# Kernel optimization log

Measured on AMD Instinct MI355X. Metric: run time of the kernel, lower is better.

## Reference

```python
import jax, jax.numpy as jnp
import numpy as np
from jax import lax

# Static model/config sizes
B, ANG, C, H, NF, NB = 1, 9, 3, 128, 16, 2


def get_freq_position(n):
    """Anti-diagonal frequency bands of an n x n angular-DCT grid (python/static)."""
    bands = []
    for i in range(n):
        bands.append(([i], [0]))
    for j in range(1, n):
        bands.append(([n - 1], [j]))
    for item in bands:
        while item[0][0] > 0 and item[1][0] < n - 1:
            item[0].insert(0, item[0][0] - 1)
            item[1].insert(0, item[1][0] + 1)
    return bands


def dct_mat(n):
    """Orthonormal DCT-II matrix (row k = k-th basis)."""
    k = jnp.arange(n, dtype=jnp.float32)[:, None]
    i = jnp.arange(n, dtype=jnp.float32)[None, :]
    m = jnp.cos(jnp.pi * (i + 0.5) * k / n) * jnp.sqrt(2.0 / n)
    return m.at[0].multiply(1.0 / np.sqrt(2.0))


def conv3d(x, w, b):
    # x: (N, Cin, D, H, W), w: (Cout, Cin, 3, 3, 3)
    y = lax.conv_general_dilated(x, w, (1, 1, 1), 'SAME',
                                 dimension_numbers=('NCDHW', 'OIDHW', 'NCDHW'))
    return y + b[None, :, None, None, None]


def branch(cut, wi, bi, a, wb, bb):
    """init conv + NB ResBlock3D (PReLU -> Conv3d, residual), plus outer skip."""
    y0 = conv3d(cut, wi, bi)
    y = y0
    for k in range(NB):
        r = jnp.where(y >= 0, y, a[k] * y)  # PReLU (single-parameter)
        y = y + conv3d(r, wb[k], bb[k])
    return y0 + y


def setup_inputs() -> dict:
    key = jax.random.key(0)
    ks = jax.random.split(key, 32)

    def nrm(k, shape, s=0.05):
        return jax.random.normal(k, shape, dtype=jnp.float32) * s

    inp = {"x": jax.random.normal(ks[0], (B, ANG, ANG, C, H, H), dtype=jnp.float32)}
    i = 1
    for n in ("dc", "lo", "mi", "hi"):
        inp[f"w_{n}_i"] = nrm(ks[i], (NF, C, 3, 3, 3)); i += 1
        inp[f"b_{n}_i"] = nrm(ks[i], (NF,)); i += 1
        inp[f"a_{n}"] = jnp.full((NB,), 0.25, dtype=jnp.float32)
        inp[f"w_{n}"] = nrm(ks[i], (NB, NF, NF, 3, 3, 3)); i += 1
        inp[f"b_{n}"] = nrm(ks[i], (NB, NF)); i += 1
    inp["w_last"] = nrm(ks[i], (C, NF))  # 1x1 Conv2d, no bias
    return inp


def reference(x, w_dc_i, b_dc_i, a_dc, w_dc, b_dc,
              w_lo_i, b_lo_i, a_lo, w_lo, b_lo,
              w_mi_i, b_mi_i, a_mi, w_mi, b_mi,
              w_hi_i, b_hi_i, a_hi, w_hi, b_hi, w_last):
    b, u, v, c, h, w = x.shape
    Da = dct_mat(u)  # angular DCT (u == v)
    Ds = dct_mat(h)  # spatial DCT (h == w)

    # SpaAngDCT: spatial 2D DCT then angular 2D DCT
    xf = jnp.einsum('buvchw,Hh,Ww->buvcHW', x, Ds, Ds)
    xf = jnp.einsum('buvchw,Uu,Vv->bUVchw', xf, Da, Da)

    x_rec = jnp.zeros((b, NF, u, v, h, w), dtype=x.dtype)
    for idx, (ui, vi) in enumerate(get_freq_position(u)):
        if idx == 0:
            p = (w_dc_i, b_dc_i, a_dc, w_dc, b_dc)
        elif idx <= 2:
            p = (w_lo_i, b_lo_i, a_lo, w_lo, b_lo)
        elif idx <= u - 1:
            p = (w_mi_i, b_mi_i, a_mi, w_mi, b_mi)
        else:
            p = (w_hi_i, b_hi_i, a_hi, w_hi, b_hi)
        ua, va = jnp.array(ui), jnp.array(vi)
        cut = xf[:, ua, va].transpose(0, 2, 1, 3, 4)  # (b, c, L, h, w)
        out = branch(cut, *p)                          # (b, NF, L, h, w)
        x_rec = x_rec.at[:, :, ua, va].set(out)        # scatter band back

    # 'b c u v h w -> b c (u h) (v w)' then 1x1 conv (NF -> 3)
    xr = x_rec.transpose(0, 1, 2, 4, 3, 5).reshape(b, NF, u * h, v * w)
    xr = jnp.einsum('bnHW,on->boHW', xr, w_last)
    xr = xr.reshape(b, c, u, h, v, w).transpose(0, 2, 4, 1, 3, 5)  # (b,u,v,c,h,w)

    # InverseSpaAngDCT: angular IDCT then spatial IDCT
    xr = jnp.einsum('bUVchw,Uu,Vv->buvchw', xr, Da, Da)
    xr = jnp.einsum('buvcHW,Hh,Ww->buvchw', xr, Ds, Ds)
    return xr + x
```

## Files before the change

### kernel.cpp

```cpp
#include <hip/hip_runtime.h>
#include <hip/hip_bf16.h>
#include <math.h>

typedef __hip_bfloat16 bf16;
typedef __attribute__((ext_vector_type(8))) short short8;
typedef __attribute__((ext_vector_type(4))) float floatx4;
typedef __attribute__((ext_vector_type(4))) unsigned int uint4v;
typedef __attribute__((ext_vector_type(2))) unsigned int uint2v;

#define HW 16384
#define NSLICE 243

__constant__ int c_s_of_p[81] = {
  0, 1,1, 2,2,2, 3,3,3,3, 4,4,4,4,4, 5,5,5,5,5,5, 6,6,6,6,6,6,6,
  7,7,7,7,7,7,7,7, 8,8,8,8,8,8,8,8,8, 9,9,9,9,9,9,9,9,
  10,10,10,10,10,10,10, 11,11,11,11,11,11, 12,12,12,12,12,
  13,13,13,13, 14,14,14, 15,15, 16};
__constant__ int c_l_of_p[81] = {
  0, 0,1, 0,1,2, 0,1,2,3, 0,1,2,3,4, 0,1,2,3,4,5, 0,1,2,3,4,5,6,
  0,1,2,3,4,5,6,7, 0,1,2,3,4,5,6,7,8, 0,1,2,3,4,5,6,7,
  0,1,2,3,4,5,6, 0,1,2,3,4,5, 0,1,2,3,4, 0,1,2,3, 0,1,2, 0,1, 0};
__constant__ int c_L_of_s[17] = {1,2,3,4,5,6,7,8,9,8,7,6,5,4,3,2,1};
__constant__ int c_g_of_s[17] = {0,1,1,2,2,2,2,2,2,3,3,3,3,3,3,3,3};
__constant__ int c_pos_uv[81] = {
  0,1,3,6,10,15,21,28,36,
  2,4,7,11,16,22,29,37,45,
  5,8,12,17,23,30,38,46,53,
  9,13,18,24,31,39,47,54,60,
  14,19,25,32,40,48,55,61,66,
  20,26,33,41,49,56,62,67,71,
  27,34,42,50,57,63,68,72,75,
  35,43,51,58,64,69,73,76,78,
  44,52,59,65,70,74,77,79,80};

struct WPtrs {
  const float* wi[4]; const float* bi[4]; const float* a[4];
  const float* wb[4]; const float* bb[4]; const float* wl;
};

__device__ __forceinline__ unsigned short f2bf(float f) {
  return __bfloat16_as_ushort(__float2bfloat16(f));
}
__device__ __forceinline__ float bf2f(unsigned short u) {
  return __uint_as_float(((unsigned int)u) << 16);
}
__device__ __forceinline__ float bflo(unsigned int w) {
  return __uint_as_float(w << 16);
}
__device__ __forceinline__ float bfhi(unsigned int w) {
  return __uint_as_float(w & 0xffff0000u);
}
__device__ __forceinline__ unsigned int pack2(float a, float b) {
  return (unsigned int)f2bf(a) | ((unsigned int)f2bf(b) << 16);
}
__device__ __forceinline__ float invprelu(float v, float invA) {
  return (v >= 0.f) ? v : v * invA;
}
__device__ __forceinline__ void bfsplit(float v, unsigned short& hi, unsigned short& lo) {
  unsigned int bits = __float_as_uint(v);
  hi = (unsigned short)(bits >> 16);
  lo = f2bf(v - __uint_as_float(bits & 0xffff0000u));
}
__device__ __forceinline__ void gl_lds16(const void* g, void* l) {
  __builtin_amdgcn_global_load_lds(
      (const __attribute__((address_space(1))) unsigned int*)g,
      (__attribute__((address_space(3))) unsigned int*)l, 16, 0, 0);
}
__device__ __forceinline__ int ldsoff(int plane, int col) {
  return plane * 2112 + ((plane & 3) << 5) + (col << 4);
}

__global__ __launch_bounds__(256) void k_init(WPtrs P, float* DaF,
                                              unsigned short* TFhi, unsigned short* TFlo,
                                              unsigned short* TIhi, unsigned short* TIlo,
                                              unsigned short* Wmf,
                                              float* BiF, float* BbF,
                                              float* AF, float* WlF) {
  const double PI = 3.14159265358979323846;
  int t = blockIdx.x * 256 + threadIdx.x;
  if (t < 81) {
    int U = t / 9, u = t % 9;
    double d = cos(PI * (u + 0.5) * U / 9.0) * sqrt(2.0 / 9.0);
    if (U == 0) d *= (1.0 / sqrt(2.0));
    DaF[t] = (float)d;
  }
  if (t < 16384) {
    int jj = t & 7, lane = (t >> 3) & 63, ks = (t >> 9) & 3, tile = t >> 11;
    int row = tile * 16 + (lane & 15);
    int colk = ks * 32 + (lane >> 4) * 8 + jj;
    double vF = cos(PI * (colk + 0.5) * row / 128.0) * sqrt(2.0 / 128.0);
    if (row == 0) vF *= (1.0 / sqrt(2.0));
    double vI = cos(PI * (row + 0.5) * colk / 128.0) * sqrt(2.0 / 128.0);
    if (colk == 0) vI *= (1.0 / sqrt(2.0));
    unsigned short h, l;
    bfsplit((float)vF, h, l); TFhi[t] = h; TFlo[t] = l;
    bfsplit((float)vI, h, l); TIhi[t] = h; TIlo[t] = l;
  }
  if (t < 92160) {
    int s = t / 7680, r = t % 7680;
    int step = r / 512, r2 = r % 512;
    int lane = r2 >> 3, j = r2 & 7;
    int d = step / 5, i = step % 5;
    int q = lane >> 4, m = lane & 15;
    int tl = 2 * i + (q >> 1);
    int cin = (q & 1) * 8 + j;
    float val = 0.f;
    if (tl <= 8) {
      int ky = tl / 3, kx = tl % 3;
      int tap = d * 9 + ky * 3 + kx;
      if (s < 4) {
        if (cin < 3) val = P.wi[s][(m * 3 + cin) * 27 + tap];
      } else {
        int g = (s - 4) >> 1, k = (s - 4) & 1;
        val = P.wb[g][((k * 16 + m) * 16 + cin) * 27 + tap];
      }
    }
    Wmf[t] = f2bf(val);
  }
  if (t < 64)  BiF[t] = P.bi[t / 16][t % 16];
  if (t < 128) BbF[t] = P.bb[t / 32][t % 32];
  if (t < 8)   AF[t]  = P.a[t / 2][t % 2];
  if (t < 48)  WlF[t] = P.wl[t];
}

__global__ __launch_bounds__(256) void k_dct2(const float* __restrict__ X,
                                              const unsigned short* __restrict__ tabhi,
                                              const unsigned short* __restrict__ tablo,
                                              const float* __restrict__ xres,
                                              float* __restrict__ Yf,
                                              unsigned short* __restrict__ Ybf) {
  __shared__ unsigned short sThi[128 * 136];
  __shared__ unsigned short sTlo[128 * 136];
  int s = blockIdx.x;
  int t = threadIdx.x;
  int lane = t & 63, wv = t >> 6;
  int q = lane >> 4, n16 = lane & 15;
  const float* Xs = X + (size_t)s * HW;

  floatx4 acc[2][8];
#pragma unroll
  for (int mt = 0; mt < 2; mt++)
#pragma unroll
    for (int nt = 0; nt < 8; nt++) acc[mt][nt] = (floatx4){0.f, 0.f, 0.f, 0.f};

#pragma unroll
  for (int ks = 0; ks < 4; ks++) {
    short8 ahi[2], alo[2];
#pragma unroll
    for (int mt = 0; mt < 2; mt++) {
      const float* xp = Xs + (wv * 32 + mt * 16 + n16) * 128 + ks * 32 + q * 8;
      float4 a = *(const float4*)xp;
      float4 b = *(const float4*)(xp + 4);
      union { short8 v; unsigned short u[8]; } H, L;
      float xv[8] = {a.x, a.y, a.z, a.w, b.x, b.y, b.z, b.w};
#pragma unroll
      for (int j = 0; j < 8; j++) bfsplit(xv[j], H.u[j], L.u[j]);
      ahi[mt] = H.v; alo[mt] = L.v;
    }
#pragma unroll
    for (int nt = 0; nt < 8; nt++) {
      int e = nt * 2048 + ks * 512 + lane * 8;
      short8 bh = *(const short8*)(tabhi + e);
      short8 bl = *(const short8*)(tablo + e);
#pragma unroll
      for (int mt = 0; mt < 2; mt++) {
        acc[mt][nt] = __builtin_amdgcn_mfma_f32_16x16x32_bf16(ahi[mt], bl, acc[mt][nt], 0, 0, 0);
        acc[mt][nt] = __builtin_amdgcn_mfma_f32_16x16x32_bf16(alo[mt], bh, acc[mt][nt], 0, 0, 0);
        acc[mt][nt] = __builtin_amdgcn_mfma_f32_16x16x32_bf16(ahi[mt], bh, acc[mt][nt], 0, 0, 0);
      }
    }
  }

#pragma unroll
  for (int mt = 0; mt < 2; mt++)
#pragma unroll
    for (int nt = 0; nt < 8; nt++) {
      int col = nt * 16 + n16;
      int rowb = wv * 32 + mt * 16 + q * 4;
#pragma unroll
      for (int rp = 0; rp < 4; rp += 2) {
        unsigned short h0, l0, h1, l1;
        bfsplit(acc[mt][nt][rp], h0, l0);
        bfsplit(acc[mt][nt][rp + 1], h1, l1);
        int widx = (col * 136 + rowb + rp) >> 1;
        ((unsigned int*)sThi)[widx] = (unsigned int)h0 | ((unsigned int)h1 << 16);
        ((unsigned int*)sTlo)[widx] = (unsigned int)l0 | ((unsigned int)l1 << 16);
      }
    }
  __syncthreads();

#pragma unroll
  for (int mt = 0; mt < 2; mt++)
#pragma unroll
    for (int nt = 0; nt < 8; nt++) acc[mt][nt] = (floatx4){0.f, 0.f, 0.f, 0.f};

#pragma unroll
  for (int ks = 0; ks < 4; ks++) {
    short8 ahi[2], alo[2];
#pragma unroll
    for (int mt = 0; mt < 2; mt++) {
      int e = (wv * 2 + mt) * 2048 + ks * 512 + lane * 8;
      ahi[mt] = *(const short8*)(tabhi + e);
      alo[mt] = *(const short8*)(tablo + e);
    }
#pragma unroll
    for (int nt = 0; nt < 8; nt++) {
      int off = (nt * 16 + n16) * 136 + ks * 32 + q * 8;
      short8 bh = *(const short8*)(sThi + off);
      short8 bl = *(const short8*)(sTlo + off);
#pragma unroll
      for (int mt = 0; mt < 2; mt++) {
        acc[mt][nt] = __builtin_amdgcn_mfma_f32_16x16x32_bf16(ahi[mt], bl, acc[mt][nt], 0, 0, 0);
        acc[mt][nt] = __builtin_amdgcn_mfma_f32_16x16x32_bf16(alo[mt], bh, acc[mt][nt], 0, 0, 0);
        acc[mt][nt] = __builtin_amdgcn_mfma_f32_16x16x32_bf16(ahi[mt], bh, acc[mt][nt], 0, 0, 0);
      }
    }
  }

#pragma unroll
  for (int mt = 0; mt < 2; mt++)
#pragma unroll
    for (int nt = 0; nt < 8; nt++) {
      int row0 = wv * 32 + mt * 16 + q * 4;
      int col = nt * 16 + n16;
#pragma unroll
      for (int r = 0; r < 4; r++) {
        size_t oi = (size_t)s * HW + (size_t)(row0 + r) * 128 + col;
        float v = acc[mt][nt][r];
        if (Ybf) {
          Ybf[oi] = f2bf(v);
        } else {
          if (xres) v += xres[oi];
          Yf[oi] = v;
        }
      }
    }
}

__global__ __launch_bounds__(256) void k_angfwd(const unsigned short* __restrict__ in,
                                                const float* __restrict__ DaF,
                                                unsigned short* __restrict__ out) {
  __shared__ float sDa[81];
  int t = threadIdx.x;
  if (t < 81) sDa[t] = DaF[t];
  __syncthreads();
  int idx = blockIdx.x * 256 + t;
  int hw = idx & (HW - 1);
  int r = idx >> 14;
  int c = r % 3, ub = r / 3;
  float tmp[3][9];
#pragma unroll
  for (int i = 0; i < 3; i++)
#pragma unroll
    for (int v = 0; v < 9; v++) tmp[i][v] = 0.f;
#pragma unroll
  for (int u = 0; u < 9; u++) {
    float fv[9];
#pragma unroll
    for (int v = 0; v < 9; v++)
      fv[v] = bf2f(in[(size_t)((u * 9 + v) * 3 + c) * HW + hw]);
#pragma unroll
    for (int i = 0; i < 3; i++) {
      float dc = sDa[(ub * 3 + i) * 9 + u];
#pragma unroll
      for (int v = 0; v < 9; v++) tmp[i][v] += dc * fv[v];
    }
  }
#pragma unroll
  for (int i = 0; i < 3; i++) {
    int U = ub * 3 + i;
#pragma unroll
    for (int V = 0; V < 9; V++) {
      float acc = 0.f;
#pragma unroll
      for (int v = 0; v < 9; v++) acc += sDa[V * 9 + v] * tmp[i][v];
      size_t base = ((size_t)c_pos_uv[U * 9 + V] * HW + hw) * 4;
      out[base + c] = f2bf(acc);
      if (c == 0) out[base + 3] = 0;
    }
  }
}

__global__ __launch_bounds__(256) void k_anginv(const float* __restrict__ xrb,
                                                const float* __restrict__ DaF,
                                                float* __restrict__ out) {
  __shared__ float sDa[81];
  int t = threadIdx.x;
  if (t < 81) sDa[t] = DaF[t];
  __syncthreads();
  int idx = blockIdx.x * 256 + t;
  int hw = idx & (HW - 1);
  int r = idx >> 14;
  int c = r % 3, ub = r / 3;
  float tmp[3][9];
#pragma unroll
  for (int i = 0; i < 3; i++)
#pragma unroll
    for (int V = 0; V < 9; V++) tmp[i][V] = 0.f;
#pragma unroll
  for (int U = 0; U < 9; U++) {
    float fV[9];
#pragma unroll
    for (int V = 0; V < 9; V++)
      fV[V] = xrb[((size_t)c_pos_uv[U * 9 + V] * 3 + c) * HW + hw];
#pragma unroll
    for (int i = 0; i < 3; i++) {
      float dc = sDa[U * 9 + (ub * 3 + i)];
#pragma unroll
      for (int V = 0; V < 9; V++) tmp[i][V] += dc * fV[V];
    }
  }
#pragma unroll
  for (int i = 0; i < 3; i++) {
    int u = ub * 3 + i;
#pragma unroll
    for (int v = 0; v < 9; v++) {
      float acc = 0.f;
#pragma unroll
      for (int V = 0; V < 9; V++) acc += sDa[V * 9 + v] * tmp[i][V];
      out[(size_t)((u * 9 + v) * 3 + c) * HW + hw] = acc;
    }
  }
}

__global__ __launch_bounds__(1024, 8) void k_conv(const unsigned short* __restrict__ src,
                                              const unsigned short* __restrict__ prevAct,
                                              const unsigned short* __restrict__ act0,
                                              const unsigned short* __restrict__ Wmf,
                                              const float* __restrict__ BiF,
                                              const float* __restrict__ BbF,
                                              const float* __restrict__ AF,
                                              const float* __restrict__ WlF,
                                              int sel,
                                              unsigned short* __restrict__ boutAct,
                                              float* __restrict__ xrbOut) {
  __shared__ unsigned short s_lds[21184];
  int p = blockIdx.y;
  int s = c_s_of_p[p], l = c_l_of_p[p];
  int g = c_g_of_s[s], Ls = c_L_of_s[s];
  int row0 = blockIdx.x * 8;
  int t = threadIdx.x;
  int lane = t & 63, wv16 = t >> 6;
  int row8 = wv16 & 7, ch = wv16 >> 3;
  int q = lane >> 4, n = lane & 15;

  float aNext = (sel < 2) ? AF[g * 2 + sel] : 0.f;
  float invA  = (sel > 0) ? 1.0f / AF[g * 2 + sel - 1] : 0.f;

  {
    uint4v z = (uint4v){0u, 0u, 0u, 0u};
    int zmax = (sel == 0) ? 1320 : 40;
    for (int i = t; i < zmax; i += 1024) {
      int row, half, col;
      if (i < 40) { row = i >> 2; half = (i >> 1) & 1; col = (i & 1) ? 129 : 0; }
      else { int j = i - 40; row = j >> 7; col = (j & 127) + 1; half = 1; }
      *(uint4v*)((char*)s_lds + ldsoff(row * 2 + half, col)) = z;
    }
    for (int row = 0; row < 10; row++) {
      int grow = row0 - 1 + row;
      if ((unsigned)grow >= 128u) {
        for (int i = t; i < 264; i += 1024) {
          int half = i / 132, col = i % 132;
          *(uint4v*)((char*)s_lds + ldsoff(row * 2 + half, col)) = z;
        }
      }
    }
  }

  int off2[5];
#pragma unroll
  for (int i = 0; i < 5; i++) {
    int tl = 2 * i + (q >> 1);
    if (tl > 8) tl = 8;
    int ky = tl / 3, kx = tl % 3;
    off2[i] = ldsoff(2 * (row8 + ky) + (q & 1), n + kx) + ch * 1024;
  }

  int setIdx = (sel == 0) ? g : (4 + g * 2 + (sel - 1));
  const char* WsetBase = (const char*)Wmf + (size_t)setIdx * 15 * 1024;

  floatx4 acc[4];
#pragma unroll
  for (int cg = 0; cg < 4; cg++) acc[cg] = (floatx4){0.f, 0.f, 0.f, 0.f};

  for (int d = 0; d < 3; d++) {
    int l2 = l + d - 1;
    if (l2 < 0 || l2 >= Ls) continue;
    int p2 = p + d - 1;
    __syncthreads();
    if (sel == 0) {
#pragma unroll
      for (int it = 0; it < 2; it++) {
        int id = t + it * 1024;
        if (id < 1280) {
          int row = id >> 7, col = id & 127;
          int grow = row0 - 1 + row;
          if ((unsigned)grow < 128u) {
            uint2v w = *(const uint2v*)(src +
                ((size_t)p2 * HW + (size_t)grow * 128 + col) * 4);
            uint4v val; val.x = w.x; val.y = w.y; val.z = 0u; val.w = 0u;
            *(uint4v*)((char*)s_lds + ldsoff(row * 2, col + 1)) = val;
          }
        }
      }
    } else {
#pragma unroll
      for (int it = 0; it < 3; it++) {
        int id = t + it * 1024;
        if (id < 2560) {
          int row = id >> 8, half = (id >> 7) & 1, col = id & 127;
          int grow = row0 - 1 + row;
          if ((unsigned)grow < 128u) {
            const void* gp = (const void*)(src +
                (((size_t)p2 * HW + (size_t)grow * 128 + col) * 16 + half * 8));
            void* lp = (void*)((char*)s_lds + ldsoff(row * 2 + half, col + 1));
            gl_lds16(gp, lp);
          }
        }
      }
    }
    __syncthreads();
    short8 af[5];
#pragma unroll
    for (int i = 0; i < 5; i++)
      af[i] = *(const short8*)(WsetBase + ((d * 5 + i) * 64 + lane) * 16);
#pragma unroll
    for (int cg = 0; cg < 4; cg++) {
#pragma unroll
      for (int i = 0; i < 5; i++) {
        short8 b = *(const short8*)((const char*)s_lds + off2[i] + cg * 256);
        acc[cg] = __builtin_amdgcn_mfma_f32_16x16x32_bf16(af[i], b, acc[cg], 0, 0, 0);
      }
    }
  }

  const float* bp = (sel == 0) ? (BiF + g * 16) : (BbF + g * 32 + (sel - 1) * 16);
  float bz[4];
#pragma unroll
  for (int r = 0; r < 4; r++) bz[r] = bp[q * 4 + r];
  int h = row0 + row8;

  if (sel < 2) {
#pragma unroll
    for (int cg = 0; cg < 4; cg++) {
      size_t pix = (size_t)p * HW + h * 128 + ch * 64 + cg * 16 + n;
      float r0 = acc[cg][0] + bz[0], r1 = acc[cg][1] + bz[1];
      float r2 = acc[cg][2] + bz[2], r3 = acc[cg][3] + bz[3];
      if (sel != 0) {
        uint2v pv = *(const uint2v*)(prevAct + pix * 16 + q * 4);
        r0 += invprelu(bflo(pv.x), invA); r1 += invprelu(bfhi(pv.x), invA);
        r2 += invprelu(bflo(pv.y), invA); r3 += invprelu(bfhi(pv.y), invA);
      }
      r0 = fmaxf(r0, 0.f) + aNext * fminf(r0, 0.f);
      r1 = fmaxf(r1, 0.f) + aNext * fminf(r1, 0.f);
      r2 = fmaxf(r2, 0.f) + aNext * fminf(r2, 0.f);
      r3 = fmaxf(r3, 0.f) + aNext * fminf(r3, 0.f);
      uint2v ov; ov.x = pack2(r0, r1); ov.y = pack2(r2, r3);
      *(uint2v*)(boutAct + pix * 16 + q * 4) = ov;
    }
  } else {
    float invA0 = 1.0f / AF[g * 2];
    float wl0[4], wl1[4], wl2[4];
#pragma unroll
    for (int r = 0; r < 4; r++) {
      wl0[r] = WlF[q * 4 + r];
      wl1[r] = WlF[16 + q * 4 + r];
      wl2[r] = WlF[32 + q * 4 + r];
    }
#pragma unroll
    for (int cg = 0; cg < 4; cg++) {
      size_t pix = (size_t)p * HW + h * 128 + ch * 64 + cg * 16 + n;
      float r0 = acc[cg][0] + bz[0], r1 = acc[cg][1] + bz[1];
      float r2 = acc[cg][2] + bz[2], r3 = acc[cg][3] + bz[3];
      uint2v pv = *(const uint2v*)(prevAct + pix * 16 + q * 4);
      r0 += invprelu(bflo(pv.x), invA); r1 += invprelu(bfhi(pv.x), invA);
      r2 += invprelu(bflo(pv.y), invA); r3 += invprelu(bfhi(pv.y), invA);
      uint2v p0 = *(const uint2v*)(act0 + pix * 16 + q * 4);
      r0 += invprelu(bflo(p0.x), invA0); r1 += invprelu(bfhi(p0.x), invA0);
      r2 += invprelu(bflo(p0.y), invA0); r3 += invprelu(bfhi(p0.y), invA0);
      float o0 = wl0[0] * r0 + wl0[1] * r1 + wl0[2] * r2 + wl0[3] * r3;
      float o1 = wl1[0] * r0 + wl1[1] * r1 + wl1[2] * r2 + wl1[3] * r3;
      float o2 = wl2[0] * r0 + wl2[1] * r1 + wl2[2] * r2 + wl2[3] * r3;
      o0 += __shfl_xor(o0, 16); o0 += __shfl_xor(o0, 32);
      o1 += __shfl_xor(o1, 16); o1 += __shfl_xor(o1, 32);
      o2 += __shfl_xor(o2, 16); o2 += __shfl_xor(o2, 32);
      if (q == 0) {
        size_t hw = (size_t)h * 128 + ch * 64 + cg * 16 + n;
        xrbOut[((size_t)p * 3 + 0) * HW + hw] = o0;
        xrbOut[((size_t)p * 3 + 1) * HW + hw] = o1;
        xrbOut[((size_t)p * 3 + 2) * HW + hw] = o2;
      }
    }
  }
}

extern "C" void kernel_launch(void* const* d_in, const int* in_sizes, int n_in,
                              void* d_out, int out_size, void* d_ws, size_t ws_size,
                              hipStream_t stream) {
  (void)in_sizes; (void)n_in; (void)out_size; (void)ws_size;
  const float* x = (const float*)d_in[0];
  WPtrs P;
  for (int g = 0; g < 4; g++) {
    int b = 1 + g * 5;
    P.wi[g] = (const float*)d_in[b + 0];
    P.bi[g] = (const float*)d_in[b + 1];
    P.a[g]  = (const float*)d_in[b + 2];
    P.wb[g] = (const float*)d_in[b + 3];
    P.bb[g] = (const float*)d_in[b + 4];
  }
  P.wl = (const float*)d_in[21];

  char* base = (char*)d_ws;
  size_t off = 0;
  auto take = [&](size_t bytes) -> char* {
    char* r = base + off;
    off += (bytes + 255) & ~(size_t)255;
    return r;
  };
  float* DaF = (float*)take(81 * 4);
  unsigned short* TFhi = (unsigned short*)take(16384 * 2);
  unsigned short* TFlo = (unsigned short*)take(16384 * 2);
  unsigned short* TIhi = (unsigned short*)take(16384 * 2);
  unsigned short* TIlo = (unsigned short*)take(16384 * 2);
  unsigned short* Wmf = (unsigned short*)take(92160 * 2);
  float* BiF   = (float*)take(256);
  float* BbF   = (float*)take(512);
  float* AF    = (float*)take(32);
  float* WlF   = (float*)take(192);
  float* R1 = (float*)take((size_t)NSLICE * HW * 4);
  unsigned short* B1 = (unsigned short*)take((size_t)NSLICE * HW * 2);
  float* R3 = (float*)take((size_t)NSLICE * HW * 4);
  unsigned short* braw0 = (unsigned short*)take((size_t)81 * 16 * HW * 2);
  unsigned short* braw1 = (unsigned short*)take((size_t)81 * 16 * HW * 2);
  unsigned short* xf2b = (unsigned short*)R3;
  float* xrb = R3;

  k_init<<<360, 256, 0, stream>>>(P, DaF, TFhi, TFlo, TIhi, TIlo,
                                  Wmf, BiF, BbF, AF, WlF);
  k_dct2<<<243, 256, 0, stream>>>(x, TFhi, TFlo, nullptr, nullptr, B1);
  k_angfwd<<<576, 256, 0, stream>>>(B1, DaF, xf2b);
  k_conv<<<dim3(16, 81), 1024, 0, stream>>>(xf2b, nullptr, nullptr, Wmf,
                                            BiF, BbF, AF, WlF, 0, braw0, nullptr);
  k_conv<<<dim3(16, 81), 1024, 0, stream>>>(braw0, braw0, nullptr, Wmf,
                                            BiF, BbF, AF, WlF, 1, braw1, nullptr);
  k_conv<<<dim3(16, 81), 1024, 0, stream>>>(braw1, braw1, braw0, Wmf,
                                            BiF, BbF, AF, WlF, 2, nullptr, xrb);
  k_anginv<<<576, 256, 0, stream>>>(xrb, DaF, R1);
  k_dct2<<<243, 256, 0, stream>>>(R1, TIhi, TIlo, x, (float*)d_out, nullptr);
}
```

Before: 278.6 us.

## Switch 3D conv from 16x16x32 MFMA to 32x32x16 MFMA with two-row output tiles

Restructures the conv inner loop to use 32x32x16 bf16 MFMA, where each wave computes two output rows times 32 columns times 16 channels. The weight matrix is re-laid-out so the M dimension covers (row offset, cout), with zero padding for invalid ky. This is meant to cut LDS B-operand reads and instruction count per FLOP. In exchange it performs 12 MFMAs per depth slice, partly on zero-padded taps, uses more accumulator registers, and lowers the launch-bounds occupancy hint.

```diff
diff --git a/kernel.cpp b/kernel.cpp
--- a/kernel.cpp
+++ b/kernel.cpp
@@ -5,6 +5,7 @@
 typedef __hip_bfloat16 bf16;
 typedef __attribute__((ext_vector_type(8))) short short8;
 typedef __attribute__((ext_vector_type(4))) float floatx4;
+typedef __attribute__((ext_vector_type(16))) float floatx16;
 typedef __attribute__((ext_vector_type(4))) unsigned int uint4v;
 typedef __attribute__((ext_vector_type(2))) unsigned int uint2v;
 
@@ -96,23 +97,25 @@
     bfsplit((float)vF, h, l); TFhi[t] = h; TFlo[t] = l;
     bfsplit((float)vI, h, l); TIhi[t] = h; TIlo[t] = l;
   }
-  if (t < 92160) {
-    int s = t / 7680, r = t % 7680;
-    int step = r / 512, r2 = r % 512;
-    int lane = r2 >> 3, j = r2 & 7;
-    int d = step / 5, i = step % 5;
-    int q = lane >> 4, m = lane & 15;
-    int tl = 2 * i + (q >> 1);
-    int cin = (q & 1) * 8 + j;
+  if (t < 221184) {
+    int j = t & 7;
+    int lane = (t >> 3) & 63;
+    int su = t >> 9;
+    int set = su / 36, r36 = su % 36;
+    int d = r36 / 12, r12 = r36 % 12;
+    int ir = r12 / 3, kx = r12 % 3;
+    int m = lane & 31, hi = lane >> 5;
+    int ror = m >> 4, cout = m & 15;
+    int cin = hi * 8 + j;
+    int ky = ir - ror;
     float val = 0.f;
-    if (tl <= 8) {
-      int ky = tl / 3, kx = tl % 3;
+    if (ky >= 0 && ky <= 2) {
       int tap = d * 9 + ky * 3 + kx;
-      if (s < 4) {
-        if (cin < 3) val = P.wi[s][(m * 3 + cin) * 27 + tap];
+      if (set < 4) {
+        if (cin < 3) val = P.wi[set][(cout * 3 + cin) * 27 + tap];
       } else {
-        int g = (s - 4) >> 1, k = (s - 4) & 1;
-        val = P.wb[g][((k * 16 + m) * 16 + cin) * 27 + tap];
+        int gg = (set - 4) >> 1, k = (set - 4) & 1;
+        val = P.wb[gg][((k * 16 + cout) * 16 + cin) * 27 + tap];
       }
     }
     Wmf[t] = f2bf(val);
@@ -323,7 +326,7 @@
   }
 }
 
-__global__ __launch_bounds__(1024, 8) void k_conv(const unsigned short* __restrict__ src,
+__global__ __launch_bounds__(1024, 4) void k_conv(const unsigned short* __restrict__ src,
                                               const unsigned short* __restrict__ prevAct,
                                               const unsigned short* __restrict__ act0,
                                               const unsigned short* __restrict__ Wmf,
@@ -340,9 +343,9 @@
   int g = c_g_of_s[s], Ls = c_L_of_s[s];
   int row0 = blockIdx.x * 8;
   int t = threadIdx.x;
-  int lane = t & 63, wv16 = t >> 6;
-  int row8 = wv16 & 7, ch = wv16 >> 3;
-  int q = lane >> 4, n = lane & 15;
+  int lane = t & 63, w = t >> 6;
+  int pr = w >> 2, cq = w & 3;
+  int m = lane & 31, hi = lane >> 5;
 
   float aNext = (sel < 2) ? AF[g * 2 + sel] : 0.f;
   float invA  = (sel > 0) ? 1.0f / AF[g * 2 + sel - 1] : 0.f;
@@ -367,21 +370,12 @@
     }
   }
 
-  int off2[5];
-#pragma unroll
-  for (int i = 0; i < 5; i++) {
-    int tl = 2 * i + (q >> 1);
-    if (tl > 8) tl = 8;
-    int ky = tl / 3, kx = tl % 3;
-    off2[i] = ldsoff(2 * (row8 + ky) + (q & 1), n + kx) + ch * 1024;
-  }
-
   int setIdx = (sel == 0) ? g : (4 + g * 2 + (sel - 1));
-  const char* WsetBase = (const char*)Wmf + (size_t)setIdx * 15 * 1024;
-
-  floatx4 acc[4];
-#pragma unroll
-  for (int cg = 0; cg < 4; cg++) acc[cg] = (floatx4){0.f, 0.f, 0.f, 0.f};
+  const char* WsetBase = (const char*)Wmf + (size_t)setIdx * 36864;
+
+  floatx16 acc;
+#pragma unroll
+  for (int r = 0; r < 16; r++) acc[r] = 0.f;
 
   for (int d = 0; d < 3; d++) {
     int l2 = l + d - 1;
@@ -396,9 +390,9 @@
           int row = id >> 7, col = id & 127;
           int grow = row0 - 1 + row;
           if ((unsigned)grow < 128u) {
-            uint2v w = *(const uint2v*)(src +
+            uint2v wv2 = *(const uint2v*)(src +
                 ((size_t)p2 * HW + (size_t)grow * 128 + col) * 4);
-            uint4v val; val.x = w.x; val.y = w.y; val.z = 0u; val.w = 0u;
+            uint4v val; val.x = wv2.x; val.y = wv2.y; val.z = 0u; val.w = 0u;
             *(uint4v*)((char*)s_lds + ldsoff(row * 2, col + 1)) = val;
           }
         }
@@ -420,75 +414,97 @@
       }
     }
     __syncthreads();
-    short8 af[5];
-#pragma unroll
-    for (int i = 0; i < 5; i++)
-      af[i] = *(const short8*)(WsetBase + ((d * 5 + i) * 64 + lane) * 16);
-#pragma unroll
-    for (int cg = 0; cg < 4; cg++) {
-#pragma unroll
-      for (int i = 0; i < 5; i++) {
-        short8 b = *(const short8*)((const char*)s_lds + off2[i] + cg * 256);
-        acc[cg] = __builtin_amdgcn_mfma_f32_16x16x32_bf16(af[i], b, acc[cg], 0, 0, 0);
+#pragma unroll
+    for (int ir = 0; ir < 4; ir++) {
+#pragma unroll
+      for (int kx = 0; kx < 3; kx++) {
+        int st = ir * 3 + kx;
+        short8 a = *(const short8*)(WsetBase +
+                     (size_t)((d * 12 + st) * 64 + lane) * 16);
+        short8 b = *(const short8*)((const char*)s_lds +
+                     ldsoff(2 * (pr * 2 + ir) + hi, cq * 32 + m + kx));
+        acc = __builtin_amdgcn_mfma_f32_32x32x16_bf16(a, b, acc, 0, 0, 0);
       }
     }
   }
 
   const float* bp = (sel == 0) ? (BiF + g * 16) : (BbF + g * 32 + (sel - 1) * 16);
-  float bz[4];
-#pragma unroll
-  for (int r = 0; r < 4; r++) bz[r] = bp[q * 4 + r];
-  int h = row0 + row8;
+  float bzA[4], bzB[4];
+#pragma unroll
+  for (int r = 0; r < 4; r++) { bzA[r] = bp[4 * hi + r]; bzB[r] = bp[8 + 4 * hi + r]; }
+  int pxcol = cq * 32 + m;
 
   if (sel < 2) {
 #pragma unroll
-    for (int cg = 0; cg < 4; cg++) {
-      size_t pix = (size_t)p * HW + h * 128 + ch * 64 + cg * 16 + n;
-      float r0 = acc[cg][0] + bz[0], r1 = acc[cg][1] + bz[1];
-      float r2 = acc[cg][2] + bz[2], r3 = acc[cg][3] + bz[3];
+    for (int ror = 0; ror < 2; ror++) {
+      int h = row0 + pr * 2 + ror;
+      size_t pix = (size_t)p * HW + h * 128 + pxcol;
+      float rA[4], rB[4];
+#pragma unroll
+      for (int j = 0; j < 4; j++) {
+        rA[j] = acc[ror * 8 + j] + bzA[j];
+        rB[j] = acc[ror * 8 + 4 + j] + bzB[j];
+      }
       if (sel != 0) {
-        uint2v pv = *(const uint2v*)(prevAct + pix * 16 + q * 4);
-        r0 += invprelu(bflo(pv.x), invA); r1 += invprelu(bfhi(pv.x), invA);
-        r2 += invprelu(bflo(pv.y), invA); r3 += invprelu(bfhi(pv.y), invA);
-      }
-      r0 = fmaxf(r0, 0.f) + aNext * fminf(r0, 0.f);
-      r1 = fmaxf(r1, 0.f) + aNext * fminf(r1, 0.f);
-      r2 = fmaxf(r2, 0.f) + aNext * fminf(r2, 0.f);
-      r3 = fmaxf(r3, 0.f) + aNext * fminf(r3, 0.f);
-      uint2v ov; ov.x = pack2(r0, r1); ov.y = pack2(r2, r3);
-      *(uint2v*)(boutAct + pix * 16 + q * 4) = ov;
+        uint2v pv = *(const uint2v*)(prevAct + pix * 16 + 4 * hi);
+        uint2v pw = *(const uint2v*)(prevAct + pix * 16 + 8 + 4 * hi);
+        rA[0] += invprelu(bflo(pv.x), invA); rA[1] += invprelu(bfhi(pv.x), invA);
+        rA[2] += invprelu(bflo(pv.y), invA); rA[3] += invprelu(bfhi(pv.y), invA);
+        rB[0] += invprelu(bflo(pw.x), invA); rB[1] += invprelu(bfhi(pw.x), invA);
+        rB[2] += invprelu(bflo(pw.y), invA); rB[3] += invprelu(bfhi(pw.y), invA);
+      }
+#pragma unroll
+      for (int j = 0; j < 4; j++) {
+        rA[j] = fmaxf(rA[j], 0.f) + aNext * fminf(rA[j], 0.f);
+        rB[j] = fmaxf(rB[j], 0.f) + aNext * fminf(rB[j], 0.f);
+      }
+      uint2v oa; oa.x = pack2(rA[0], rA[1]); oa.y = pack2(rA[2], rA[3]);
+      uint2v ob; ob.x = pack2(rB[0], rB[1]); ob.y = pack2(rB[2], rB[3]);
+      *(uint2v*)(boutAct + pix * 16 + 4 * hi) = oa;
+      *(uint2v*)(boutAct + pix * 16 + 8 + 4 * hi) = ob;
     }
   } else {
     float invA0 = 1.0f / AF[g * 2];
-    float wl0[4], wl1[4], wl2[4];
-#pragma unroll
-    for (int r = 0; r < 4; r++) {
-      wl0[r] = WlF[q * 4 + r];
-      wl1[r] = WlF[16 + q * 4 + r];
-      wl2[r] = WlF[32 + q * 4 + r];
-    }
-#pragma unroll
-    for (int cg = 0; cg < 4; cg++) {
-      size_t pix = (size_t)p * HW + h * 128 + ch * 64 + cg * 16 + n;
-      float r0 = acc[cg][0] + bz[0], r1 = acc[cg][1] + bz[1];
-      float r2 = acc[cg][2] + bz[2], r3 = acc[cg][3] + bz[3];
-      uint2v pv = *(const uint2v*)(prevAct + pix * 16 + q * 4);
-      r0 += invprelu(bflo(pv.x), invA); r1 += invprelu(bfhi(pv.x), invA);
-      r2 += invprelu(bflo(pv.y), invA); r3 += invprelu(bfhi(pv.y), invA);
-      uint2v p0 = *(const uint2v*)(act0 + pix * 16 + q * 4);
-      r0 += invprelu(bflo(p0.x), invA0); r1 += invprelu(bfhi(p0.x), invA0);
-      r2 += invprelu(bflo(p0.y), invA0); r3 += invprelu(bfhi(p0.y), invA0);
-      float o0 = wl0[0] * r0 + wl0[1] * r1 + wl0[2] * r2 + wl0[3] * r3;
-      float o1 = wl1[0] * r0 + wl1[1] * r1 + wl1[2] * r2 + wl1[3] * r3;
-      float o2 = wl2[0] * r0 + wl2[1] * r1 + wl2[2] * r2 + wl2[3] * r3;
-      o0 += __shfl_xor(o0, 16); o0 += __shfl_xor(o0, 32);
-      o1 += __shfl_xor(o1, 16); o1 += __shfl_xor(o1, 32);
-      o2 += __shfl_xor(o2, 16); o2 += __shfl_xor(o2, 32);
-      if (q == 0) {
-        size_t hw = (size_t)h * 128 + ch * 64 + cg * 16 + n;
-        xrbOut[((size_t)p * 3 + 0) * HW + hw] = o0;
-        xrbOut[((size_t)p * 3 + 1) * HW + hw] = o1;
-        xrbOut[((size_t)p * 3 + 2) * HW + hw] = o2;
+    float4 wlA[3], wlB[3];
+#pragma unroll
+    for (int c = 0; c < 3; c++) {
+      wlA[c] = *(const float4*)(WlF + c * 16 + 4 * hi);
+      wlB[c] = *(const float4*)(WlF + c * 16 + 8 + 4 * hi);
+    }
+#pragma unroll
+    for (int ror = 0; ror < 2; ror++) {
+      int h = row0 + pr * 2 + ror;
+      size_t pix = (size_t)p * HW + h * 128 + pxcol;
+      float rA[4], rB[4];
+#pragma unroll
+      for (int j = 0; j < 4; j++) {
+        rA[j] = acc[ror * 8 + j] + bzA[j];
+        rB[j] = acc[ror * 8 + 4 + j] + bzB[j];
+      }
+      uint2v pv = *(const uint2v*)(prevAct + pix * 16 + 4 * hi);
+      uint2v pw = *(const uint2v*)(prevAct + pix * 16 + 8 + 4 * hi);
+      rA[0] += invprelu(bflo(pv.x), invA); rA[1] += invprelu(bfhi(pv.x), invA);
+      rA[2] += invprelu(bflo(pv.y), invA); rA[3] += invprelu(bfhi(pv.y), invA);
+      rB[0] += invprelu(bflo(pw.x), invA); rB[1] += invprelu(bfhi(pw.x), invA);
+      rB[2] += invprelu(bflo(pw.y), invA); rB[3] += invprelu(bfhi(pw.y), invA);
+      uint2v qv = *(const uint2v*)(act0 + pix * 16 + 4 * hi);
+      uint2v qw = *(const uint2v*)(act0 + pix * 16 + 8 + 4 * hi);
+      rA[0] += invprelu(bflo(qv.x), invA0); rA[1] += invprelu(bfhi(qv.x), invA0);
+      rA[2] += invprelu(bflo(qv.y), invA0); rA[3] += invprelu(bfhi(qv.y), invA0);
+      rB[0] += invprelu(bflo(qw.x), invA0); rB[1] += invprelu(bfhi(qw.x), invA0);
+      rB[2] += invprelu(bflo(qw.y), invA0); rB[3] += invprelu(bfhi(qw.y), invA0);
+      float o[3];
+#pragma unroll
+      for (int c = 0; c < 3; c++) {
+        o[c] = wlA[c].x * rA[0] + wlA[c].y * rA[1] + wlA[c].z * rA[2] + wlA[c].w * rA[3]
+             + wlB[c].x * rB[0] + wlB[c].y * rB[1] + wlB[c].z * rB[2] + wlB[c].w * rB[3];
+        o[c] += __shfl_xor(o[c], 32);
+      }
+      if (hi == 0) {
+        size_t hw = (size_t)h * 128 + pxcol;
+        xrbOut[((size_t)p * 3 + 0) * HW + hw] = o[0];
+        xrbOut[((size_t)p * 3 + 1) * HW + hw] = o[1];
+        xrbOut[((size_t)p * 3 + 2) * HW + hw] = o[2];
       }
     }
   }
@@ -522,7 +538,7 @@
   unsigned short* TFlo = (unsigned short*)take(16384 * 2);
   unsigned short* TIhi = (unsigned short*)take(16384 * 2);
   unsigned short* TIlo = (unsigned short*)take(16384 * 2);
-  unsigned short* Wmf = (unsigned short*)take(92160 * 2);
+  unsigned short* Wmf = (unsigned short*)take(221184 * 2);
   float* BiF   = (float*)take(256);
   float* BbF   = (float*)take(512);
   float* AF    = (float*)take(32);
@@ -535,7 +551,7 @@
   unsigned short* xf2b = (unsigned short*)R3;
   float* xrb = R3;
 
-  k_init<<<360, 256, 0, stream>>>(P, DaF, TFhi, TFlo, TIhi, TIlo,
+  k_init<<<864, 256, 0, stream>>>(P, DaF, TFhi, TFlo, TIhi, TIlo,
                                   Wmf, BiF, BbF, AF, WlF);
   k_dct2<<<243, 256, 0, stream>>>(x, TFhi, TFlo, nullptr, nullptr, B1);
   k_angfwd<<<576, 256, 0, stream>>>(B1, DaF, xf2b);
```

Result: slower. 311.8 us (+11.9%).
